# Performance work log

Measured on AMD Instinct MI355X. Metric: run time of the kernel, lower is better.

The kernel has to match this reference:

```python
import jax, jax.numpy as jnp
import numpy as np

SR = 22050
FMIN = 220.0
N_BINS = 84
BPO = 12
HOP = 512
NORM_P = 1
T_SAMPLES = 8388608  # 2**23 samples of audio


def _make_kernels():
    Q = 1.0 / (2.0 ** (1.0 / BPO) - 1.0)
    fftLen = 2 ** int(np.ceil(np.log2(np.ceil(Q * SR / FMIN))))  # 2048
    freqs = FMIN * 2.0 ** (np.arange(N_BINS) / float(BPO))
    temp = np.zeros((N_BINS, fftLen), dtype=np.complex64)
    for k in range(N_BINS):
        freq = freqs[k]
        l = np.ceil(Q * SR / freq)
        if l % 2 == 1:
            start = int(np.ceil(fftLen / 2.0 - l / 2.0)) - 1
        else:
            start = int(np.ceil(fftLen / 2.0 - l / 2.0))
        li = int(l)
        n = np.arange(li)
        hann = 0.5 - 0.5 * np.cos(2 * np.pi * n / li)  # periodic ('fftbins=True') hann
        idx = np.arange(np.floor(-l / 2.0), np.floor(l / 2.0))
        temp[k, start:start + li] = hann * np.exp(1j * 2 * np.pi * freq / SR * idx) / li
    spec = np.fft.fft(temp, axis=1)[:, : fftLen // 2 + 1]
    kr = spec.real.astype(np.float32)
    ki = spec.imag.astype(np.float32)
    # norm=1 branch: divide by L1 norm (over bins axis, dim=0) of complex magnitude
    mag = np.sqrt(kr ** 2 + ki ** 2)
    denom = np.sum(np.abs(mag), axis=0)  # shape [freq_bins]
    kr = (kr / denom).astype(np.float32)
    ki = (ki / denom).astype(np.float32)
    # Fourier kernels: freq_scale='no', windowing='no'
    freq_bins = fftLen // 2 + 1
    s = np.arange(fftLen, dtype=np.float64)
    kk = np.arange(freq_bins, dtype=np.float64)
    ang = 2 * np.pi * np.outer(kk, s) / fftLen  # [freq_bins, fftLen]
    wsin = np.sin(ang).astype(np.float32)
    wcos = np.cos(ang).astype(np.float32)
    return kr, ki, wcos, wsin


def setup_inputs() -> dict:
    key = jax.random.key(0)
    x = jax.random.normal(key, (T_SAMPLES,), dtype=jnp.float32)
    kr, ki, wcos, wsin = _make_kernels()
    return {
        "x": x,
        "wcos": jnp.asarray(wcos),
        "wsin": jnp.asarray(wsin),
        "kr": jnp.asarray(kr),
        "ki": jnp.asarray(ki),
    }


def reference(x, wcos, wsin, kr, ki):
    fftLen = wcos.shape[1]  # 2048
    n_frames = (x.shape[0] - fftLen) // HOP + 1  # static under jit
    # frame the signal: equivalent to conv1d(x, w, stride=HOP) with kernels w
    idx = jnp.arange(n_frames)[:, None] * HOP + jnp.arange(fftLen)[None, :]
    frames = x[idx]  # [n_frames, fftLen]
    fourier_real = jnp.einsum("fn,kn->kf", frames, wcos)  # [freq_bins, n_frames]
    fourier_imag = jnp.einsum("fn,kn->kf", frames, wsin)
    cqt_real = kr @ fourier_real - ki @ fourier_imag  # [n_bins, n_frames]
    cqt_imag = kr @ fourier_imag + ki @ fourier_real
    cqt = jnp.sqrt(cqt_real ** 2 + cqt_imag ** 2)
    return cqt[None]  # [1, n_bins, n_frames]
```

## Files before the change

kernel.cpp:

```cpp
#include <hip/hip_runtime.h>


#define HOPS 512
#define NBINS 84
#define FREQB 1025
#define NFRAMES 16381
#define TSAMP 8388608
#define SPAN 34304
#define KP16 138

typedef short bf16x8 __attribute__((ext_vector_type(8)));
typedef float f32x16 __attribute__((ext_vector_type(16)));

union B8 { struct { ushort4 lo, hi; } p; bf16x8 v; uint4 u; };

__device__ __forceinline__ unsigned short f32_to_bf16(float f) {
    union { float f; unsigned u; } v; v.f = f;
    return (unsigned short)((v.u + 0x7FFFu + ((v.u >> 16) & 1u)) >> 16);
}
__device__ __forceinline__ unsigned pk_bf16(float lo, float hi) {
    return (unsigned)f32_to_bf16(lo) | ((unsigned)f32_to_bf16(hi) << 16);
}
__device__ __forceinline__ bf16x8 pack8(const float* s) {
    B8 r;
    r.u.x = pk_bf16(s[0], s[1]); r.u.y = pk_bf16(s[2], s[3]);
    r.u.z = pk_bf16(s[4], s[5]); r.u.w = pk_bf16(s[6], s[7]);
    return r.v;
}

__device__ __forceinline__ float cos_rev(float r) { return __builtin_amdgcn_cosf(r); }
__device__ __forceinline__ float sin_rev(float r) { return __builtin_amdgcn_sinf(r); }

__global__ __launch_bounds__(64) void aprep_kernel(
    const float* __restrict__ kr, const float* __restrict__ ki,
    unsigned short* __restrict__ Apf)
{
    const int bid = blockIdx.x;
    const int row = bid / 5, c = bid % 5;
    const int l = threadIdx.x;
    const int q = c * 64 + l;
    if (q >= 276) return;

    const int b = row >> 1, im = row & 1;
    const bool bok = b < NBINS;
    const float* cosp = (im ? ki : kr) + (size_t)(bok ? b : 0) * FREQB;
    const float* sinp = (im ? kr : ki) + (size_t)(bok ? b : 0) * FREQB;
    const float ssign = im ? 1.f : -1.f;

    const int k0 = q * 8;
    unsigned short o[8];
    #pragma unroll
    for (int j = 0; j < 8; ++j) {
        int k = k0 + j;
        float v = 0.f;
        if (bok) {
            if (k <= 1024)       v = cosp[k];
            else if (k <= 2049)  v = ssign * sinp[k - 1025];
        }
        o[j] = f32_to_bf16(v);
    }
    uint4 pk;
    pk.x = (unsigned)o[0] | ((unsigned)o[1] << 16);
    pk.y = (unsigned)o[2] | ((unsigned)o[3] << 16);
    pk.z = (unsigned)o[4] | ((unsigned)o[5] << 16);
    pk.w = (unsigned)o[6] | ((unsigned)o[7] << 16);

    const int mt = row >> 5, c32 = row & 31;
    const int k16 = q >> 1, h = q & 1;
    *(uint4*)(Apf + (size_t)(mt * KP16 + k16) * 512 + (size_t)(h * 32 + c32) * 8) = pk;
}

__global__ __launch_bounds__(512) void wfused_kernel(
    const unsigned short* __restrict__ Apf, unsigned short* __restrict__ Wpf)
{
    __shared__ float4 red[7][4][64];

    const int bid = blockIdx.x;
    const int mt = bid >> 6, nt = bid & 63;
    const int t = threadIdx.x;
    const int w = t >> 6, l = t & 63;
    const int c32 = l & 31, h = l >> 5;
    const int n = nt * 32 + c32;

    f32x16 acc;
    #pragma unroll
    for (int i = 0; i < 16; ++i) acc[i] = 0.f;

    const int k0 = (w == 0) ? 0 : 16 * w + 1;
    const int kcnt = (w == 0) ? 17 : 16;
    const unsigned short* ap = Apf + (size_t)(mt * KP16 + k0) * 512 + (size_t)l * 8;

    for (int i = 0; i < kcnt; ++i) {
        const int k16 = k0 + i;
        B8 bf; bf.u = *(const uint4*)(ap + (size_t)i * 512);
        float tv[8];
        const int kb = k16 * 16 + h * 8;
        if (k16 <= 63) {
            #pragma unroll
            for (int j = 0; j < 8; ++j) {
                int p = __mul24(kb + j, n) & 2047;
                tv[j] = cos_rev((float)p * (1.f / 2048.f));
            }
        } else if (k16 >= 65 && k16 <= 127) {
            #pragma unroll
            for (int j = 0; j < 8; ++j) {
                int p = __mul24(kb + j - 1025, n) & 2047;
                tv[j] = sin_rev((float)p * (1.f / 2048.f));
            }
        } else {
            #pragma unroll
            for (int j = 0; j < 8; ++j) {
                int k = kb + j;
                float v = 0.f;
                if (k <= 1024) {
                    int p = __mul24(k, n) & 2047;
                    v = cos_rev((float)p * (1.f / 2048.f));
                } else if (k <= 2049) {
                    int p = __mul24(k - 1025, n) & 2047;
                    v = sin_rev((float)p * (1.f / 2048.f));
                }
                tv[j] = v;
            }
        }
        acc = __builtin_amdgcn_mfma_f32_32x32x16_bf16(pack8(tv), bf.v, acc, 0, 0, 0);
    }

    if (w > 0) {
        #pragma unroll
        for (int q = 0; q < 4; ++q)
            red[w - 1][q][l] = make_float4(acc[4*q+0], acc[4*q+1], acc[4*q+2], acc[4*q+3]);
    }
    __syncthreads();
    if (w == 0) {
        #pragma unroll
        for (int s = 0; s < 7; ++s) {
            #pragma unroll
            for (int q = 0; q < 4; ++q) {
                float4 v = red[s][q][l];
                acc[4*q+0] += v.x; acc[4*q+1] += v.y;
                acc[4*q+2] += v.z; acc[4*q+3] += v.w;
            }
        }
        #pragma unroll
        for (int g = 0; g < 4; ++g) {
            uint2 qo;
            qo.x = pk_bf16(acc[4*g+0], acc[4*g+1]);
            qo.y = pk_bf16(acc[4*g+2], acc[4*g+3]);
            size_t off = (size_t)(mt * 128 + nt * 2 + (g >> 1)) * 512
                       + (size_t)(c32 + 32 * (g & 1)) * 8 + 4 * h;
            *(uint2*)(Wpf + off) = qo;
        }
    }
}

__global__ __launch_bounds__(768) void cqt_kernel(
    const float* __restrict__ x, const unsigned short* __restrict__ Wpf,
    float* __restrict__ out)
{
    __shared__ __align__(16) unsigned short xl[SPAN];

    const int t = threadIdx.x;
    const int f0 = blockIdx.x * 64;
    const long S0 = (long)f0 * HOPS;
    const int valid = (int)((TSAMP - S0) < (long)SPAN ? (TSAMP - S0) : (long)SPAN);

    #pragma unroll
    for (int i = 0; i < 12; ++i) {
        int idx4 = t + i * 768;
        if (idx4 < 8576) {
            int s = idx4 * 4;
            float4 v = make_float4(0.f, 0.f, 0.f, 0.f);
            if (s + 4 <= valid) v = *(const float4*)(x + S0 + s);
            ushort4 o;
            o.x = f32_to_bf16(v.x); o.y = f32_to_bf16(v.y);
            o.z = f32_to_bf16(v.z); o.w = f32_to_bf16(v.w);
            int byte = idx4 * 8;
            int bsw = byte ^ (((byte >> 10) & 7) << 4);
            *(ushort4*)((char*)xl + bsw) = o;
        }
    }
    __syncthreads();

    const int w = t >> 6, l = t & 63;
    const int mg = w >> 1, fg = w & 1;
    const int c32 = l & 31, h = l >> 5;

    const unsigned short* apf = Wpf + (size_t)mg * (128 * 512) + (size_t)l * 8;
    const int byteBase = (fg * 32 + c32) * 1024 + h * 16;

    f32x16 acc;
    #pragma unroll
    for (int i = 0; i < 16; ++i) acc[i] = 0.f;

    auto ldsB = [&](int k16) -> bf16x8 {
        int byte = byteBase + k16 * 32;
        int bsw = byte ^ (((byte >> 10) & 7) << 4);
        B8 r;
        r.u = *(const uint4*)((const char*)xl + bsw);
        return r.v;
    };

    uint4 Abuf[2][8];
    #pragma unroll
    for (int j = 0; j < 8; ++j)
        Abuf[0][j] = *(const uint4*)(apf + (size_t)j * 512);

    #pragma unroll
    for (int c = 0; c < 16; ++c) {
        const int cur = c & 1, nxt = cur ^ 1;
        if (c < 15) {
            #pragma unroll
            for (int j = 0; j < 8; ++j)
                Abuf[nxt][j] = *(const uint4*)(apf + (size_t)((c + 1) * 8 + j) * 512);
        }
        #pragma unroll
        for (int j = 0; j < 8; ++j) {
            B8 af; af.u = Abuf[cur][j];
            acc = __builtin_amdgcn_mfma_f32_32x32x16_bf16(af.v, ldsB(c * 8 + j), acc, 0, 0, 0);
        }
    }

    const int f = f0 + fg * 32 + c32;
    if (f < NFRAMES) {
        #pragma unroll
        for (int rp = 0; rp < 4; ++rp) {
            int base = mg * 32 + 8 * rp + 4 * h;
            int b0 = base >> 1;
            float r0 = acc[4 * rp + 0], i0 = acc[4 * rp + 1];
            float r1 = acc[4 * rp + 2], i1 = acc[4 * rp + 3];
            if (b0 < NBINS)
                out[(size_t)b0 * NFRAMES + f] = sqrtf(r0 * r0 + i0 * i0);
            if (b0 + 1 < NBINS)
                out[(size_t)(b0 + 1) * NFRAMES + f] = sqrtf(r1 * r1 + i1 * i1);
        }
    }
}

extern "C" void kernel_launch(void* const* d_in, const int* in_sizes, int n_in,
                              void* d_out, int out_size, void* d_ws, size_t ws_size,
                              hipStream_t stream) {
    const float* x    = (const float*)d_in[0];
    const float* kr   = (const float*)d_in[3];
    const float* ki   = (const float*)d_in[4];
    float* out = (float*)d_out;

    unsigned short* Wpf = (unsigned short*)d_ws;
    unsigned short* Apf = (unsigned short*)((char*)d_ws + 786432);

    aprep_kernel<<<dim3(960), dim3(64), 0, stream>>>(kr, ki, Apf);
    wfused_kernel<<<dim3(384), dim3(512), 0, stream>>>(Apf, Wpf);
    cqt_kernel<<<dim3(256), dim3(768), 0, stream>>>(x, Wpf, out);
}
```

Measured before the change: 118.9 us.

## Fuse three kernels into one cooperative kernel with grid syncs

Merges the kernel-matrix prep, the fused DFT·CQT weight GEMM, and the main CQT GEMM into a single cooperative launch of 256 blocks, using grid.sync between phases. This removes two kernel launches and their inter-kernel gaps. The weight GEMM now splits K across 12 waves instead of 8 and loops over 384 tiles with 256 blocks. That leaves an imbalanced second pass, and the grid barriers plus the shared 68KB LDS may limit occupancy.

New measurement: 302.1 us. +154.2%, slower.

```diff
diff --git a/kernel.cpp b/kernel.cpp
--- a/kernel.cpp
+++ b/kernel.cpp
@@ -1,4 +1,7 @@
 #include <hip/hip_runtime.h>
+#include <hip/hip_cooperative_groups.h>
+
+namespace cg = cooperative_groups;
 
 
 #define HOPS 512
@@ -31,207 +34,216 @@
 __device__ __forceinline__ float cos_rev(float r) { return __builtin_amdgcn_cosf(r); }
 __device__ __forceinline__ float sin_rev(float r) { return __builtin_amdgcn_sinf(r); }
 
-__global__ __launch_bounds__(64) void aprep_kernel(
+__global__ __launch_bounds__(768) void cqt_all_kernel(
+    const float* __restrict__ x,
     const float* __restrict__ kr, const float* __restrict__ ki,
-    unsigned short* __restrict__ Apf)
+    unsigned short* __restrict__ Apf, unsigned short* __restrict__ Wpf,
+    float* __restrict__ out)
 {
+    __shared__ __align__(16) char lds[68608];
+    unsigned short* xl = (unsigned short*)lds;
+    float4 (*red)[4][64] = (float4 (*)[4][64])lds;
+
+    const int t = threadIdx.x;
     const int bid = blockIdx.x;
-    const int row = bid / 5, c = bid % 5;
-    const int l = threadIdx.x;
-    const int q = c * 64 + l;
-    if (q >= 276) return;
-
-    const int b = row >> 1, im = row & 1;
-    const bool bok = b < NBINS;
-    const float* cosp = (im ? ki : kr) + (size_t)(bok ? b : 0) * FREQB;
-    const float* sinp = (im ? kr : ki) + (size_t)(bok ? b : 0) * FREQB;
-    const float ssign = im ? 1.f : -1.f;
-
-    const int k0 = q * 8;
-    unsigned short o[8];
-    #pragma unroll
-    for (int j = 0; j < 8; ++j) {
-        int k = k0 + j;
-        float v = 0.f;
-        if (bok) {
-            if (k <= 1024)       v = cosp[k];
-            else if (k <= 2049)  v = ssign * sinp[k - 1025];
-        }
-        o[j] = f32_to_bf16(v);
+    cg::grid_group grid = cg::this_grid();
+
+    {
+        const int gid = bid * 768 + t;
+        if (gid < 192 * 320) {
+            const int row = gid / 320;
+            const int q = gid % 320;
+            if (q < 276) {
+                const int b = row >> 1, im = row & 1;
+                const bool bok = b < NBINS;
+                const float* cosp = (im ? ki : kr) + (size_t)(bok ? b : 0) * FREQB;
+                const float* sinp = (im ? kr : ki) + (size_t)(bok ? b : 0) * FREQB;
+                const float ssign = im ? 1.f : -1.f;
+                const int k0 = q * 8;
+                unsigned short o[8];
+                #pragma unroll
+                for (int j = 0; j < 8; ++j) {
+                    int k = k0 + j;
+                    float v = 0.f;
+                    if (bok) {
+                        if (k <= 1024)       v = cosp[k];
+                        else if (k <= 2049)  v = ssign * sinp[k - 1025];
+                    }
+                    o[j] = f32_to_bf16(v);
+                }
+                uint4 pk;
+                pk.x = (unsigned)o[0] | ((unsigned)o[1] << 16);
+                pk.y = (unsigned)o[2] | ((unsigned)o[3] << 16);
+                pk.z = (unsigned)o[4] | ((unsigned)o[5] << 16);
+                pk.w = (unsigned)o[6] | ((unsigned)o[7] << 16);
+                const int mt = row >> 5, c32r = row & 31;
+                const int k16 = q >> 1, hh = q & 1;
+                *(uint4*)(Apf + (size_t)(mt * KP16 + k16) * 512
+                              + (size_t)(hh * 32 + c32r) * 8) = pk;
+            }
+        }
     }
-    uint4 pk;
-    pk.x = (unsigned)o[0] | ((unsigned)o[1] << 16);
-    pk.y = (unsigned)o[2] | ((unsigned)o[3] << 16);
-    pk.z = (unsigned)o[4] | ((unsigned)o[5] << 16);
-    pk.w = (unsigned)o[6] | ((unsigned)o[7] << 16);
-
-    const int mt = row >> 5, c32 = row & 31;
-    const int k16 = q >> 1, h = q & 1;
-    *(uint4*)(Apf + (size_t)(mt * KP16 + k16) * 512 + (size_t)(h * 32 + c32) * 8) = pk;
-}
-
-__global__ __launch_bounds__(512) void wfused_kernel(
-    const unsigned short* __restrict__ Apf, unsigned short* __restrict__ Wpf)
-{
-    __shared__ float4 red[7][4][64];
-
-    const int bid = blockIdx.x;
-    const int mt = bid >> 6, nt = bid & 63;
-    const int t = threadIdx.x;
-    const int w = t >> 6, l = t & 63;
-    const int c32 = l & 31, h = l >> 5;
-    const int n = nt * 32 + c32;
-
-    f32x16 acc;
-    #pragma unroll
-    for (int i = 0; i < 16; ++i) acc[i] = 0.f;
-
-    const int k0 = (w == 0) ? 0 : 16 * w + 1;
-    const int kcnt = (w == 0) ? 17 : 16;
-    const unsigned short* ap = Apf + (size_t)(mt * KP16 + k0) * 512 + (size_t)l * 8;
-
-    for (int i = 0; i < kcnt; ++i) {
-        const int k16 = k0 + i;
-        B8 bf; bf.u = *(const uint4*)(ap + (size_t)i * 512);
-        float tv[8];
-        const int kb = k16 * 16 + h * 8;
-        if (k16 <= 63) {
+    __threadfence();
+    grid.sync();
+
+    {
+        const int w = t >> 6, l = t & 63;
+        const int c32 = l & 31, h = l >> 5;
+        for (int tile = bid; tile < 384; tile += 256) {
+            const int mt = tile >> 6, nt = tile & 63;
+            const int n = nt * 32 + c32;
+
+            f32x16 acc;
+            #pragma unroll
+            for (int i = 0; i < 16; ++i) acc[i] = 0.f;
+
+            const int k0 = (w < 9) ? w * 11 : 99 + (w - 9) * 10;
+            const int kcnt = (w < 9) ? 11 : 10;
+            const unsigned short* ap = Apf + (size_t)(mt * KP16 + k0) * 512
+                                           + (size_t)l * 8;
+
+            for (int i = 0; i < kcnt; ++i) {
+                const int k16 = k0 + i;
+                B8 bf; bf.u = *(const uint4*)(ap + (size_t)i * 512);
+                float tv[8];
+                const int kb = k16 * 16 + h * 8;
+                if (k16 <= 63) {
+                    #pragma unroll
+                    for (int j = 0; j < 8; ++j) {
+                        int p = __mul24(kb + j, n) & 2047;
+                        tv[j] = cos_rev((float)p * (1.f / 2048.f));
+                    }
+                } else if (k16 >= 65 && k16 <= 127) {
+                    #pragma unroll
+                    for (int j = 0; j < 8; ++j) {
+                        int p = __mul24(kb + j - 1025, n) & 2047;
+                        tv[j] = sin_rev((float)p * (1.f / 2048.f));
+                    }
+                } else {
+                    #pragma unroll
+                    for (int j = 0; j < 8; ++j) {
+                        int k = kb + j;
+                        float v = 0.f;
+                        if (k <= 1024) {
+                            int p = __mul24(k, n) & 2047;
+                            v = cos_rev((float)p * (1.f / 2048.f));
+                        } else if (k <= 2049) {
+                            int p = __mul24(k - 1025, n) & 2047;
+                            v = sin_rev((float)p * (1.f / 2048.f));
+                        }
+                        tv[j] = v;
+                    }
+                }
+                acc = __builtin_amdgcn_mfma_f32_32x32x16_bf16(pack8(tv), bf.v, acc, 0, 0, 0);
+            }
+
+            if (w > 0) {
+                #pragma unroll
+                for (int q = 0; q < 4; ++q)
+                    red[w - 1][q][l] = make_float4(acc[4*q+0], acc[4*q+1],
+                                                   acc[4*q+2], acc[4*q+3]);
+            }
+            __syncthreads();
+            if (w == 0) {
+                #pragma unroll
+                for (int s = 0; s < 11; ++s) {
+                    #pragma unroll
+                    for (int q = 0; q < 4; ++q) {
+                        float4 v = red[s][q][l];
+                        acc[4*q+0] += v.x; acc[4*q+1] += v.y;
+                        acc[4*q+2] += v.z; acc[4*q+3] += v.w;
+                    }
+                }
+                #pragma unroll
+                for (int g = 0; g < 4; ++g) {
+                    uint2 qo;
+                    qo.x = pk_bf16(acc[4*g+0], acc[4*g+1]);
+                    qo.y = pk_bf16(acc[4*g+2], acc[4*g+3]);
+                    size_t off = (size_t)(mt * 128 + nt * 2 + (g >> 1)) * 512
+                               + (size_t)(c32 + 32 * (g & 1)) * 8 + 4 * h;
+                    *(uint2*)(Wpf + off) = qo;
+                }
+            }
+            __syncthreads();
+        }
+    }
+    __threadfence();
+    grid.sync();
+
+    {
+        const int f0 = bid * 64;
+        const long S0 = (long)f0 * HOPS;
+        const int valid = (int)((TSAMP - S0) < (long)SPAN ? (TSAMP - S0) : (long)SPAN);
+
+        #pragma unroll
+        for (int i = 0; i < 12; ++i) {
+            int idx4 = t + i * 768;
+            if (idx4 < 8576) {
+                int s = idx4 * 4;
+                float4 v = make_float4(0.f, 0.f, 0.f, 0.f);
+                if (s + 4 <= valid) v = *(const float4*)(x + S0 + s);
+                ushort4 o;
+                o.x = f32_to_bf16(v.x); o.y = f32_to_bf16(v.y);
+                o.z = f32_to_bf16(v.z); o.w = f32_to_bf16(v.w);
+                int byte = idx4 * 8;
+                int bsw = byte ^ (((byte >> 10) & 7) << 4);
+                *(ushort4*)((char*)xl + bsw) = o;
+            }
+        }
+        __syncthreads();
+
+        const int w = t >> 6, l = t & 63;
+        const int mg = w >> 1, fg = w & 1;
+        const int c32 = l & 31, h = l >> 5;
+
+        const unsigned short* apf = Wpf + (size_t)mg * (128 * 512) + (size_t)l * 8;
+        const int byteBase = (fg * 32 + c32) * 1024 + h * 16;
+
+        f32x16 acc;
+        #pragma unroll
+        for (int i = 0; i < 16; ++i) acc[i] = 0.f;
+
+        auto ldsB = [&](int k16) -> bf16x8 {
+            int byte = byteBase + k16 * 32;
+            int bsw = byte ^ (((byte >> 10) & 7) << 4);
+            B8 r;
+            r.u = *(const uint4*)((const char*)xl + bsw);
+            return r.v;
+        };
+
+        uint4 Abuf[2][8];
+        #pragma unroll
+        for (int j = 0; j < 8; ++j)
+            Abuf[0][j] = *(const uint4*)(apf + (size_t)j * 512);
+
+        #pragma unroll
+        for (int c = 0; c < 16; ++c) {
+            const int cur = c & 1, nxt = cur ^ 1;
+            if (c < 15) {
+                #pragma unroll
+                for (int j = 0; j < 8; ++j)
+                    Abuf[nxt][j] = *(const uint4*)(apf + (size_t)((c + 1) * 8 + j) * 512);
+            }
             #pragma unroll
             for (int j = 0; j < 8; ++j) {
-                int p = __mul24(kb + j, n) & 2047;
-                tv[j] = cos_rev((float)p * (1.f / 2048.f));
-            }
-        } else if (k16 >= 65 && k16 <= 127) {
+                B8 af; af.u = Abuf[cur][j];
+                acc = __builtin_amdgcn_mfma_f32_32x32x16_bf16(af.v, ldsB(c * 8 + j), acc, 0, 0, 0);
+            }
+        }
+
+        const int f = f0 + fg * 32 + c32;
+        if (f < NFRAMES) {
             #pragma unroll
-            for (int j = 0; j < 8; ++j) {
-                int p = __mul24(kb + j - 1025, n) & 2047;
-                tv[j] = sin_rev((float)p * (1.f / 2048.f));
-            }
-        } else {
-            #pragma unroll
-            for (int j = 0; j < 8; ++j) {
-                int k = kb + j;
-                float v = 0.f;
-                if (k <= 1024) {
-                    int p = __mul24(k, n) & 2047;
-                    v = cos_rev((float)p * (1.f / 2048.f));
-                } else if (k <= 2049) {
-                    int p = __mul24(k - 1025, n) & 2047;
-                    v = sin_rev((float)p * (1.f / 2048.f));
-                }
-                tv[j] = v;
-            }
-        }
-        acc = __builtin_amdgcn_mfma_f32_32x32x16_bf16(pack8(tv), bf.v, acc, 0, 0, 0);
-    }
-
-    if (w > 0) {
-        #pragma unroll
-        for (int q = 0; q < 4; ++q)
-            red[w - 1][q][l] = make_float4(acc[4*q+0], acc[4*q+1], acc[4*q+2], acc[4*q+3]);
-    }
-    __syncthreads();
-    if (w == 0) {
-        #pragma unroll
-        for (int s = 0; s < 7; ++s) {
-            #pragma unroll
-            for (int q = 0; q < 4; ++q) {
-                float4 v = red[s][q][l];
-                acc[4*q+0] += v.x; acc[4*q+1] += v.y;
-                acc[4*q+2] += v.z; acc[4*q+3] += v.w;
-            }
-        }
-        #pragma unroll
-        for (int g = 0; g < 4; ++g) {
-            uint2 qo;
-            qo.x = pk_bf16(acc[4*g+0], acc[4*g+1]);
-            qo.y = pk_bf16(acc[4*g+2], acc[4*g+3]);
-            size_t off = (size_t)(mt * 128 + nt * 2 + (g >> 1)) * 512
-                       + (size_t)(c32 + 32 * (g & 1)) * 8 + 4 * h;
-            *(uint2*)(Wpf + off) = qo;
-        }
-    }
-}
-
-__global__ __launch_bounds__(768) void cqt_kernel(
-    const float* __restrict__ x, const unsigned short* __restrict__ Wpf,
-    float* __restrict__ out)
-{
-    __shared__ __align__(16) unsigned short xl[SPAN];
-
-    const int t = threadIdx.x;
-    const int f0 = blockIdx.x * 64;
-    const long S0 = (long)f0 * HOPS;
-    const int valid = (int)((TSAMP - S0) < (long)SPAN ? (TSAMP - S0) : (long)SPAN);
-
-    #pragma unroll
-    for (int i = 0; i < 12; ++i) {
-        int idx4 = t + i * 768;
-        if (idx4 < 8576) {
-            int s = idx4 * 4;
-            float4 v = make_float4(0.f, 0.f, 0.f, 0.f);
-            if (s + 4 <= valid) v = *(const float4*)(x + S0 + s);
-            ushort4 o;
-            o.x = f32_to_bf16(v.x); o.y = f32_to_bf16(v.y);
-            o.z = f32_to_bf16(v.z); o.w = f32_to_bf16(v.w);
-            int byte = idx4 * 8;
-            int bsw = byte ^ (((byte >> 10) & 7) << 4);
-            *(ushort4*)((char*)xl + bsw) = o;
-        }
-    }
-    __syncthreads();
-
-    const int w = t >> 6, l = t & 63;
-    const int mg = w >> 1, fg = w & 1;
-    const int c32 = l & 31, h = l >> 5;
-
-    const unsigned short* apf = Wpf + (size_t)mg * (128 * 512) + (size_t)l * 8;
-    const int byteBase = (fg * 32 + c32) * 1024 + h * 16;
-
-    f32x16 acc;
-    #pragma unroll
-    for (int i = 0; i < 16; ++i) acc[i] = 0.f;
-
-    auto ldsB = [&](int k16) -> bf16x8 {
-        int byte = byteBase + k16 * 32;
-        int bsw = byte ^ (((byte >> 10) & 7) << 4);
-        B8 r;
-        r.u = *(const uint4*)((const char*)xl + bsw);
-        return r.v;
-    };
-
-    uint4 Abuf[2][8];
-    #pragma unroll
-    for (int j = 0; j < 8; ++j)
-        Abuf[0][j] = *(const uint4*)(apf + (size_t)j * 512);
-
-    #pragma unroll
-    for (int c = 0; c < 16; ++c) {
-        const int cur = c & 1, nxt = cur ^ 1;
-        if (c < 15) {
-            #pragma unroll
-            for (int j = 0; j < 8; ++j)
-                Abuf[nxt][j] = *(const uint4*)(apf + (size_t)((c + 1) * 8 + j) * 512);
-        }
-        #pragma unroll
-        for (int j = 0; j < 8; ++j) {
-            B8 af; af.u = Abuf[cur][j];
-            acc = __builtin_amdgcn_mfma_f32_32x32x16_bf16(af.v, ldsB(c * 8 + j), acc, 0, 0, 0);
-        }
-    }
-
-    const int f = f0 + fg * 32 + c32;
-    if (f < NFRAMES) {
-        #pragma unroll
-        for (int rp = 0; rp < 4; ++rp) {
-            int base = mg * 32 + 8 * rp + 4 * h;
-            int b0 = base >> 1;
-            float r0 = acc[4 * rp + 0], i0 = acc[4 * rp + 1];
-            float r1 = acc[4 * rp + 2], i1 = acc[4 * rp + 3];
-            if (b0 < NBINS)
-                out[(size_t)b0 * NFRAMES + f] = sqrtf(r0 * r0 + i0 * i0);
-            if (b0 + 1 < NBINS)
-                out[(size_t)(b0 + 1) * NFRAMES + f] = sqrtf(r1 * r1 + i1 * i1);
+            for (int rp = 0; rp < 4; ++rp) {
+                int base = mg * 32 + 8 * rp + 4 * h;
+                int b0 = base >> 1;
+                float r0 = acc[4 * rp + 0], i0 = acc[4 * rp + 1];
+                float r1 = acc[4 * rp + 2], i1 = acc[4 * rp + 3];
+                if (b0 < NBINS)
+                    out[(size_t)b0 * NFRAMES + f] = sqrtf(r0 * r0 + i0 * i0);
+                if (b0 + 1 < NBINS)
+                    out[(size_t)(b0 + 1) * NFRAMES + f] = sqrtf(r1 * r1 + i1 * i1);
+            }
         }
     }
 }
@@ -247,7 +259,8 @@
     unsigned short* Wpf = (unsigned short*)d_ws;
     unsigned short* Apf = (unsigned short*)((char*)d_ws + 786432);
 
-    aprep_kernel<<<dim3(960), dim3(64), 0, stream>>>(kr, ki, Apf);
-    wfused_kernel<<<dim3(384), dim3(512), 0, stream>>>(Apf, Wpf);
-    cqt_kernel<<<dim3(256), dim3(768), 0, stream>>>(x, Wpf, out);
-}
+    void* args[] = { (void*)&x, (void*)&kr, (void*)&ki,
+                     (void*)&Apf, (void*)&Wpf, (void*)&out };
+    hipLaunchCooperativeKernel((void*)cqt_all_kernel, dim3(256), dim3(768),
+                               args, 0, stream);
+}
```
